# Kernel tuning notes

Hardware: AMD Instinct MI355X
Metric: run time of the kernel (lower is better)

The kernel has to match this reference:

```python
import jax, jax.numpy as jnp
import numpy as np

TOKEN_BITS = 10
CODEBOOK_SIZE = 2 ** TOKEN_BITS
COMMITMENT_COST = 0.25
ENT_WEIGHT = 0.1
ENT_TEMP = 0.01
ENT_GAMMA = 1.0
EPS = 1e-5


def _make_codebook():
    bits_to_indices = 2 ** np.arange(TOKEN_BITS, dtype=np.int64)  # [c]
    all_codes = np.arange(CODEBOOK_SIZE, dtype=np.int64)  # [n]
    bits = ((all_codes[:, None] & bits_to_indices) != 0).astype(np.float32)
    return jnp.asarray(bits * 2.0 - 1.0)  # [n, c] in {-1, +1}


def setup_inputs() -> dict:
    key = jax.random.key(0)
    z = jax.random.normal(key, (64, 10, 32, 32), dtype=jnp.float32)  # [b, c, h, w]
    codebook = _make_codebook()  # [1024, 10]
    return {"z": z, "codebook": codebook}


def reference(z, codebook):
    # b c h w -> b h w c
    zc = jnp.transpose(z, (0, 2, 3, 1))
    # strategy == 'default': sign quantization to {-1, +1}
    z_hard = jnp.where(zc > 0.0, 1.0, -1.0).astype(zc.dtype)

    # bit-pack indices (bits represented by sign)
    bits_to_indices = (2 ** jnp.arange(TOKEN_BITS, dtype=jnp.int32))  # [c]
    min_encoding_indices = jnp.sum((zc > 0.0).astype(jnp.int32) * bits_to_indices, axis=-1)  # [b, h, w]

    # entropy loss (ent_strategy == 'default', training mode)
    d = -2.0 * jnp.einsum('bhwc,nc->bhwn', zc, codebook)
    affinity = (-d).reshape(-1, CODEBOOK_SIZE) / ENT_TEMP  # [bhw, n]
    probs = jax.nn.softmax(affinity, axis=-1)
    log_probs = jax.nn.log_softmax(affinity + EPS, axis=-1)
    per_sample_entropy = -jnp.mean(jnp.sum(probs * log_probs, axis=-1))
    avg_probs = jnp.mean(probs, axis=0)  # [n]
    avg_entropy = -jnp.sum(avg_probs * jnp.log(avg_probs + EPS)) * ENT_GAMMA
    entropy_loss = ENT_WEIGHT * (per_sample_entropy - avg_entropy)

    # straight-through estimator
    z_q = zc + jax.lax.stop_gradient(z_hard - zc)
    commitment_loss = COMMITMENT_COST * jnp.mean((jax.lax.stop_gradient(z_q) - zc) ** 2)
    loss = commitment_loss + entropy_loss

    z_q_out = jnp.transpose(z_q, (0, 3, 1, 2))  # b h w c -> b c h w
    return (z_q_out, loss, commitment_loss, entropy_loss,
            per_sample_entropy, avg_entropy, min_encoding_indices)
```

## Files before the change

kernel.cpp:

```cpp
#include <hip/hip_runtime.h>
#include <math.h>

#define NPIX    65536
#define NELEM   655360
#define NCODE   1024
#define CSTRIDE 1024
#define BSTRIDE 10240
#define NBLK    256
#define NHB     16

#define SOFT_T 0.22f

#define WS_HIST 0
#define WS_PLP  (NBLK * NCODE)
#define WS_COM  (WS_PLP + NBLK)
#define WS_ENT  (WS_COM + NBLK)
#define WS_TKT  (WS_ENT + NHB)


__global__ void __launch_bounds__(256)
k_pixel(const float* __restrict__ z,
        float* __restrict__ zq,
        float* __restrict__ out_idx,
        float* __restrict__ ws) {
    __shared__ float hist[NCODE];
    __shared__ uint4 s_e[256 * 11];
    __shared__ float2 red[256];

    int tid = threadIdx.x;
    if (blockIdx.x == 0 && tid == 0) ((unsigned*)ws)[WS_TKT] = 0u;

    for (int i = tid; i < NCODE; i += 256) hist[i] = 0.f;
    __syncthreads();

    int p = blockIdx.x * 256 + tid;
    int b = p >> 10;
    int hw = p & 1023;
    const float* zp = z  + b * BSTRIDE + hw;
    float*       qp = zq + b * BSTRIDE + hw;
    uint4* et = &s_e[tid * 11];

    int idx = 0, k = 0;
    float commit = 0.f;
    float Z = 1.f, W = 0.f;
#pragma unroll
    for (int c = 0; c < 10; ++c) {
        float x = zp[c * CSTRIDE];
        float h = (x > 0.f) ? 1.f : -1.f;
        qp[c * CSTRIDE] = h;
        float d = h - x;
        commit = fmaf(d, d, commit);
        if (x > 0.f) idx |= (1 << c);
        float a = fabsf(x);
        float t = -400.f * a;
        float e = __expf(t);
        float op = 1.f + e;
        Z *= op;
        W = fmaf(t, e * __builtin_amdgcn_rcpf(op), W);
        if (a < SOFT_T) {
            uint4 u;
            u.x = __float_as_uint(e);
            u.y = __float_as_uint(__expf(-t));
            u.z = 1u << c;
            u.w = 0u;
            et[k] = u; ++k;
        }
    }
    out_idx[p] = (float)idx;
    float invZ = __builtin_amdgcn_rcpf(Z);
    float plogp = W - __logf(Z);

    uint4 e0 = et[0], e1 = et[1], e2 = et[2], e3 = et[3];
    float E0 = __uint_as_float(e0.x), I0 = __uint_as_float(e0.y);
    float E1 = __uint_as_float(e1.x), I1 = __uint_as_float(e1.y);
    float E2 = __uint_as_float(e2.x), I2 = __uint_as_float(e2.y);
    float E3 = __uint_as_float(e3.x), I3 = __uint_as_float(e3.y);
    unsigned M0 = e0.z, M1 = e1.z, M2 = e2.z, M3 = e3.z;

    int nsub = 1 << k;
    atomicAdd(&hist[idx], invZ);

    float w = invZ;
    unsigned cm = 0, gray = 0;
    uint4 hi = et[4];
    for (int j = 0, mb = 0; mb + 1 < nsub; mb += 16, ++j) {
        uint4 hin = et[(__ffs(j + 2) - 1) + 4];
        float f3 = (j & 1) ? I3 : E3;
#define STEP(S, FCT, MSK)                                            \
        if (mb + (S) < nsub) {                                       \
            w *= (FCT); cm ^= (MSK);                                 \
            atomicAdd(&hist[idx ^ cm], w);                           \
        }
        STEP(1,  E0, M0)
        STEP(2,  E1, M1)
        STEP(3,  I0, M0)
        STEP(4,  E2, M2)
        STEP(5,  E0, M0)
        STEP(6,  I1, M1)
        STEP(7,  I0, M0)
        STEP(8,  f3, M3)
        STEP(9,  E0, M0)
        STEP(10, E1, M1)
        STEP(11, I0, M0)
        STEP(12, I2, M2)
        STEP(13, E0, M0)
        STEP(14, I1, M1)
        STEP(15, I0, M0)
#undef STEP
        if (mb + 16 < nsub) {
            unsigned bb = 1u << ((__ffs(j + 1) - 1) + 4);
            gray ^= bb;
            float fh = (gray & bb) ? __uint_as_float(hi.x)
                                   : __uint_as_float(hi.y);
            w *= fh; cm ^= hi.z;
            atomicAdd(&hist[idx ^ cm], w);
        }
        hi = hin;
    }

    red[tid] = make_float2(plogp, commit);
    __syncthreads();
    for (int st = 128; st > 0; st >>= 1) {
        if (tid < st) {
            red[tid].x += red[tid + st].x;
            red[tid].y += red[tid + st].y;
        }
        __syncthreads();
    }
    if (tid == 0) {
        ws[WS_PLP + blockIdx.x] = red[0].x;
        ws[WS_COM + blockIdx.x] = red[0].y;
    }

    float4* hc = (float4*)(ws + WS_HIST + (size_t)blockIdx.x * NCODE);
    float4* hs = (float4*)hist;
    hc[tid] = hs[tid];
}

__global__ void __launch_bounds__(1024)
k_final(const float* __restrict__ ws_r, float* __restrict__ ws,
        float* __restrict__ out_sc) {
    __shared__ float sh[16 * 64];
    __shared__ float2 red[256];
    __shared__ int s_tkt;

    int t = threadIdx.x;
    int lane = t & 63;
    int w = t >> 6;
    int bin = blockIdx.x * 64 + lane;
    float acc = 0.f;
#pragma unroll 4
    for (int c = w; c < NBLK; c += 16)
        acc += ws_r[WS_HIST + (size_t)c * NCODE + bin];
    sh[w * 64 + lane] = acc;
    __syncthreads();
    if (t < 64) {
        float a = sh[lane];
#pragma unroll
        for (int g = 1; g < 16; ++g) a += sh[g * 64 + lane];
        a *= (1.f / 65536.f);
        float ent = -a * __logf(a + 1e-5f);
#pragma unroll
        for (int off = 32; off > 0; off >>= 1)
            ent += __shfl_down(ent, off, 64);
        if (lane == 0) {
            ws[WS_ENT + blockIdx.x] = ent;
            s_tkt = (int)__hip_atomic_fetch_add((unsigned*)ws + WS_TKT, 1u,
                                                __ATOMIC_ACQ_REL,
                                                __HIP_MEMORY_SCOPE_AGENT);
        }
    }
    __syncthreads();
    if (s_tkt != NHB - 1) return;

    if (t < 256) red[t] = make_float2(ws_r[WS_PLP + t], ws_r[WS_COM + t]);
    __syncthreads();
    for (int st = 128; st > 0; st >>= 1) {
        if (t < st) {
            red[t].x += red[t + st].x;
            red[t].y += red[t + st].y;
        }
        __syncthreads();
    }
    if (t == 0) {
        float avg_entropy = 0.f;
#pragma unroll
        for (int g = 0; g < NHB; ++g) avg_entropy += ws[WS_ENT + g];
        float pse = -red[0].x * (1.f / 65536.f);
        float cl  = 0.25f * red[0].y * (1.f / (float)NELEM);
        float el  = 0.1f * (pse - avg_entropy);
        out_sc[0] = cl + el;
        out_sc[1] = cl;
        out_sc[2] = el;
        out_sc[3] = pse;
        out_sc[4] = avg_entropy;
    }
}

extern "C" void kernel_launch(void* const* d_in, const int* in_sizes, int n_in,
                              void* d_out, int out_size, void* d_ws, size_t ws_size,
                              hipStream_t stream) {
    const float* z = (const float*)d_in[0];
    float* out = (float*)d_out;
    float* ws = (float*)d_ws;

    k_pixel<<<NBLK, 256, 0, stream>>>(z, out, out + NELEM + 5, ws);
    k_final<<<NHB, 1024, 0, stream>>>(ws, ws, out + NELEM);
}
```

Before: 71.68 us.

## Split each pixel's subset enumeration across two threads, doubling block count

Each pixel is now handled by two threads. They split the enumeration of soft-bit subsets on the last soft bit, so each walks half of the Gray-code sequence. The grid doubles to 512 blocks of 128 pixels, and only the first thread of each pair writes outputs and reduction terms. The aim is to shorten the serial per-thread histogram loop and raise occupancy, at the cost of loading z twice, running the exp work twice and making the final kernel's histogram reduction twice as large.

```diff
diff --git a/kernel.cpp b/kernel.cpp
--- a/kernel.cpp
+++ b/kernel.cpp
@@ -6,7 +6,7 @@
 #define NCODE   1024
 #define CSTRIDE 1024
 #define BSTRIDE 10240
-#define NBLK    256
+#define NBLK    512
 #define NHB     16
 
 #define SOFT_T 0.22f
@@ -33,9 +33,10 @@
     for (int i = tid; i < NCODE; i += 256) hist[i] = 0.f;
     __syncthreads();
 
-    int p = blockIdx.x * 256 + tid;
-    int b = p >> 10;
-    int hw = p & 1023;
+    int r = tid >> 7;
+    int pid = blockIdx.x * 128 + (tid & 127);
+    int b = pid >> 10;
+    int hw = pid & 1023;
     const float* zp = z  + b * BSTRIDE + hw;
     float*       qp = zq + b * BSTRIDE + hw;
     uint4* et = &s_e[tid * 11];
@@ -43,11 +44,12 @@
     int idx = 0, k = 0;
     float commit = 0.f;
     float Z = 1.f, W = 0.f;
+    float lastE = 0.f; unsigned lastM = 0u;
 #pragma unroll
     for (int c = 0; c < 10; ++c) {
         float x = zp[c * CSTRIDE];
         float h = (x > 0.f) ? 1.f : -1.f;
-        qp[c * CSTRIDE] = h;
+        if (r == 0) qp[c * CSTRIDE] = h;
         float d = h - x;
         commit = fmaf(d, d, commit);
         if (x > 0.f) idx |= (1 << c);
@@ -64,9 +66,10 @@
             u.z = 1u << c;
             u.w = 0u;
             et[k] = u; ++k;
-        }
-    }
-    out_idx[p] = (float)idx;
+            lastE = e; lastM = u.z;
+        }
+    }
+    if (r == 0) out_idx[pid] = (float)idx;
     float invZ = __builtin_amdgcn_rcpf(Z);
     float plogp = W - __logf(Z);
 
@@ -77,10 +80,15 @@
     float E3 = __uint_as_float(e3.x), I3 = __uint_as_float(e3.y);
     unsigned M0 = e0.z, M1 = e1.z, M2 = e2.z, M3 = e3.z;
 
-    int nsub = 1 << k;
-    atomicAdd(&hist[idx], invZ);
+    int kk = (k > 0) ? (k - 1) : 0;
+    int nsub = 1 << kk;
+    bool active = (r == 0) || (k > 0);
 
     float w = invZ;
+    int hidx = idx;
+    if (r == 1) { w *= lastE; hidx ^= lastM; }
+    if (active) atomicAdd(&hist[hidx], w);
+
     unsigned cm = 0, gray = 0;
     uint4 hi = et[4];
     for (int j = 0, mb = 0; mb + 1 < nsub; mb += 16, ++j) {
@@ -89,7 +97,7 @@
 #define STEP(S, FCT, MSK)                                            \
         if (mb + (S) < nsub) {                                       \
             w *= (FCT); cm ^= (MSK);                                 \
-            atomicAdd(&hist[idx ^ cm], w);                           \
+            atomicAdd(&hist[hidx ^ cm], w);                          \
         }
         STEP(1,  E0, M0)
         STEP(2,  E1, M1)
@@ -113,12 +121,12 @@
             float fh = (gray & bb) ? __uint_as_float(hi.x)
                                    : __uint_as_float(hi.y);
             w *= fh; cm ^= hi.z;
-            atomicAdd(&hist[idx ^ cm], w);
+            atomicAdd(&hist[hidx ^ cm], w);
         }
         hi = hin;
     }
 
-    red[tid] = make_float2(plogp, commit);
+    red[tid] = (r == 0) ? make_float2(plogp, commit) : make_float2(0.f, 0.f);
     __syncthreads();
     for (int st = 128; st > 0; st >>= 1) {
         if (tid < st) {
@@ -173,7 +181,9 @@
     __syncthreads();
     if (s_tkt != NHB - 1) return;
 
-    if (t < 256) red[t] = make_float2(ws_r[WS_PLP + t], ws_r[WS_COM + t]);
+    if (t < 256)
+        red[t] = make_float2(ws_r[WS_PLP + t] + ws_r[WS_PLP + 256 + t],
+                             ws_r[WS_COM + t] + ws_r[WS_COM + 256 + t]);
     __syncthreads();
     for (int st = 128; st > 0; st >>= 1) {
         if (t < st) {
```

Result: no change. 71.18 us (-0.7%).
